# Kernel tuning notes

Hardware: AMD Instinct MI355X
Metric: run time of the kernel (lower is better)

## Reference

```python
import jax, jax.numpy as jnp
import numpy as np

T, V, E, H = 512, 32000, 512, 512

def setup_inputs() -> dict:
    key = jax.random.key(0)
    ks = jax.random.split(key, 6)
    return {
        "sent": jax.random.normal(ks[0], (T, V), dtype=jnp.float32),
        "W_e": jax.random.normal(ks[1], (E, V), dtype=jnp.float32),
        "W_x": jax.random.normal(ks[2], (H, E), dtype=jnp.float32),
        "W_h": jax.random.normal(ks[3], (H, H), dtype=jnp.float32),
        "W_p": jax.random.normal(ks[4], (V, H), dtype=jnp.float32),
        "b": jax.random.normal(ks[5], (H,), dtype=jnp.float32),
    }

def reference(sent, W_e, W_x, W_h, W_p, b):
    # Embed all input words at once (embed_word: W_e @ word), skip last token.
    emb = sent[:-1] @ W_e.T                 # [T-1, E]
    xproj = emb @ W_x.T + b                 # [T-1, H] (W_x @ e + b precomputed)

    def step(h_prev, xp):
        h = jax.nn.sigmoid(xp + W_h @ h_prev)  # elman_unit
        return h, h

    h0 = jnp.zeros((H,), dtype=jnp.float32)
    _, hs = jax.lax.scan(step, h0, xproj)   # [T-1, H]
    logits = hs @ W_p.T                     # [T-1, V]
    preds = jax.nn.softmax(logits, axis=-1) # softmax over vocab (dim=0 per step)
    return preds
```

## Files before the change

kernel.cpp:

```cpp
#include <hip/hip_runtime.h>
#include <math.h>

#define ROWS 511
#define VV   32000
#define HH   512

#define SLOTF   3584
#define DARRCAP 26112
#define TBL     520
#define MAXQ    17

__device__ __forceinline__ int pad4not8(int x) {
    int p = (x + 3) & ~3;
    if ((p & 7) == 0) p += 4;
    return p;
}
__device__ __forceinline__ int pad4(int x) { return (x + 3) & ~3; }

__device__ __forceinline__ int rfl(int x) { return __builtin_amdgcn_readfirstlane(x); }

__global__ __launch_bounds__(256) void gemm_nt(
    const float* __restrict__ A, const float* __restrict__ B, float* __restrict__ C,
    int M, int lda, int ldb, int ldc, int kChunk, int useAtomic)
{
    __shared__ float As[16][68];
    __shared__ float Bs[16][68];
    const int tid = threadIdx.x;
    const int bn = blockIdx.x, bm = blockIdx.y, bz = blockIdx.z;
    const int row = tid >> 2;
    const int seg = (tid & 3) << 2;
    const int tm  = (tid >> 4) << 2;
    const int tn  = (tid & 15) << 2;
    const int am = bm*64 + row;
    const size_t k0 = (size_t)bz * kChunk;
    const float* Ap = A + (size_t)am*lda + k0 + seg;
    const float* Bp = B + (size_t)(bn*64 + row)*ldb + k0 + seg;
    const bool aok = (am < M);
    float acc[4][4];
#pragma unroll
    for (int i=0;i<4;i++)
#pragma unroll
        for (int j=0;j<4;j++) acc[i][j]=0.f;

    for (int kt = 0; kt < kChunk; kt += 16) {
        float4 av = aok ? *(const float4*)(Ap + kt) : make_float4(0.f,0.f,0.f,0.f);
        float4 bv = *(const float4*)(Bp + kt);
        __syncthreads();
        As[seg+0][row]=av.x; As[seg+1][row]=av.y; As[seg+2][row]=av.z; As[seg+3][row]=av.w;
        Bs[seg+0][row]=bv.x; Bs[seg+1][row]=bv.y; Bs[seg+2][row]=bv.z; Bs[seg+3][row]=bv.w;
        __syncthreads();
#pragma unroll
        for (int k=0;k<16;k++){
            const float4 a  = *(const float4*)&As[k][tm];
            const float4 b4 = *(const float4*)&Bs[k][tn];
            float ar[4]={a.x,a.y,a.z,a.w};
            float br[4]={b4.x,b4.y,b4.z,b4.w};
#pragma unroll
            for (int i=0;i<4;i++)
#pragma unroll
                for (int j=0;j<4;j++)
                    acc[i][j] += ar[i]*br[j];
        }
    }
#pragma unroll
    for (int i=0;i<4;i++){
        int gm = bm*64 + tm + i;
        if (gm < M) {
            float* Cp = C + (size_t)gm*ldc + bn*64 + tn;
            if (useAtomic) {
                atomicAdd(Cp+0, acc[i][0]); atomicAdd(Cp+1, acc[i][1]);
                atomicAdd(Cp+2, acc[i][2]); atomicAdd(Cp+3, acc[i][3]);
            } else {
                *(float4*)Cp = make_float4(acc[i][0],acc[i][1],acc[i][2],acc[i][3]);
            }
        }
    }
}

__global__ __launch_bounds__(64) void rsum_kernel(const float* __restrict__ W_h, float* __restrict__ R)
{
    const int j = blockIdx.x;
    const int lane = threadIdx.x;
    float s = 0.f;
    for (int i = lane; i < HH; i += 64) s += fabsf(W_h[(size_t)j*HH + i]);
#pragma unroll
    for (int off = 32; off >= 1; off >>= 1) s += __shfl_down(s, off);
    if (lane == 0) R[j] = s;
}

__global__ __launch_bounds__(512) void classify_kernel(
    float* __restrict__ xp, const float* __restrict__ b, const float* __restrict__ R,
    float* __restrict__ Hm, int* __restrict__ idxJ, int* __restrict__ cnt)
{
    const int t = blockIdx.x;
    const int j = threadIdx.x;
    __shared__ int c;
    if (j == 0) c = 0;
    __syncthreads();
    float v = xp[(size_t)t*HH + j] + b[j];
    xp[(size_t)t*HH + j] = v;
    Hm[(size_t)t*HH + j] = (v > 0.f) ? 1.f : 0.f;
    if (fabsf(v) < R[j] + 30.0f) {
        int slot = atomicAdd(&c, 1);
        if (slot < 128) idxJ[t*128 + slot] = j;
    }
    __syncthreads();
    if (j == 0) cnt[t] = (c < 128) ? c : 128;
}

__global__ __launch_bounds__(512) void prefix_kernel(
    const int* __restrict__ cnt, int* __restrict__ offs, int* __restrict__ d4offs)
{
    __shared__ int sA[512];
    __shared__ int sB[512];
    const int t = threadIdx.x;
    int a = 0, b = 0;
    if (t >= 1 && t <= 510) a = cnt[t] * pad4not8(cnt[t-1]);
    if (t <= 510) b = pad4(cnt[t]);
    sA[t] = a; sB[t] = b;
    int va = a, vb = b;
    __syncthreads();
    for (int d = 1; d < 512; d <<= 1) {
        int ua = (t >= d) ? sA[t-d] : 0;
        int ub = (t >= d) ? sB[t-d] : 0;
        __syncthreads();
        va += ua; vb += ub;
        sA[t] = va; sB[t] = vb;
        __syncthreads();
    }
    if (t <= 510) offs[t] = va - a;
    d4offs[t] = vb - b;
}

__global__ __launch_bounds__(256) void gather_kernel(
    const float* __restrict__ W_h, const float* __restrict__ xp, const float* __restrict__ U,
    const int* __restrict__ idxJ, const int* __restrict__ cnt, const int* __restrict__ offs,
    float* __restrict__ wsub, int wsub_cap, float2* __restrict__ zs)
{
    const int t = blockIdx.x;
    const int cj = cnt[t];
    for (int jj = threadIdx.x; jj < cj; jj += 256) {
        int j = idxJ[t*128 + jj];
        float xpv = xp[(size_t)t*HH + j];
        float v = xpv;
        if (t > 0) v += U[(size_t)(t-1)*HH + j];
        zs[t*128 + jj] = make_float2(v, (xpv > 0.f) ? 1.f : 0.f);
    }
    if (t == 0) return;
    const int ci  = cnt[t-1];
    const int cip = pad4not8(ci);
    const int nw  = cj * cip;
    const int base = offs[t];
    if (base + nw > wsub_cap) return;
    for (int r = 0; r < cj; ++r) {
        const float* Wrow = W_h + (size_t)idxJ[t*128 + r] * HH;
        for (int c = threadIdx.x; c < cip; c += 256)
            wsub[base + r*cip + c] = (c < ci) ? Wrow[idxJ[(t-1)*128 + c]] : 0.f;
    }
}

__global__ __launch_bounds__(64, 1) void scan_kernel(
    const float2* __restrict__ zs, const int* __restrict__ idxJ,
    const int* __restrict__ cnt, const int* __restrict__ offs, const int* __restrict__ d4offs,
    const float* __restrict__ wsub, int wsub_cap,
    const float* __restrict__ W_h, float* __restrict__ Hm, float* __restrict__ darrg)
{
    __shared__ __align__(16) float  darr[DARRCAP];
    __shared__ __align__(16) float  db[2][132];
    __shared__ __align__(16) int4   rec[TBL];
    const int lane = threadIdx.x;
    const float* zsf = (const float*)zs;

    for (int i = lane; i < TBL; i += 64) {
        int c = (i < ROWS) ? cnt[i]    : 0;
        int o = (i < ROWS) ? offs[i]   : 0;
        int d = (i < ROWS) ? d4offs[i] : d4offs[511];
        rec[i] = make_int4(c, o, d, 0);
    }
    for (int i = lane * 4; i < DARRCAP; i += 256)
        *(float4*)&darr[i] = make_float4(0.f, 0.f, 0.f, 0.f);
    for (int i = lane; i < 132; i += 64) { db[0][i] = 0.f; db[1][i] = 0.f; }
    __syncthreads();

    const int  total   = rfl(rec[511].z);
    const bool useDarr = (total <= DARRCAP - 64);

    {
        const int cj0 = rfl(rec[0].x);
        for (int jj = lane; jj < cj0; jj += 64) {
            float2 zz = zs[jj];
            float h = 1.f / (1.f + __expf(-zz.x));
            float d = h - zz.y;
            if (useDarr) darr[jj] = d;
            else { db[0][jj] = d; Hm[idxJ[jj]] = h; }
        }
    }

    float4 W0[MAXQ], W1[MAXQ], W2[MAXQ];
    float2 z0, z1, z2;

    int ciP, sd4P;
    int cjC, sd4C, n4C; bool fastC;
    int cjN, sd4N, n4N; bool fastN;
    int cj2, wb2, sd42;

#define PF(CJPREV, CJT, WBT, BANK, ZB, TT, N4OUT, FASTOUT) do {                 \
        int cip_ = pad4not8(CJPREV);                                            \
        N4OUT = cip_ >> 2;                                                      \
        FASTOUT = ((CJT) <= 64) && (cip_ <= 68) &&                              \
                  ((long)(CJT) * cip_ <= SLOTF) && ((WBT) + SLOTF <= wsub_cap); \
        int row_ = min(lane, max((CJT) - 1, 0));                                \
        const float* gW_ = wsub + (FASTOUT ? ((WBT) + row_ * cip_) : 0);        \
        _Pragma("unroll")                                                       \
        for (int q = 0; q < MAXQ; ++q) {                                        \
            int off_ = (q < N4OUT) ? (q << 2) : 0;                              \
            BANK[q] = *(const float4*)(gW_ + off_);                             \
        }                                                                       \
        ZB = *(const float2*)&zsf[(size_t)(TT) * 256 + (lane << 1)];            \
    } while (0)

#define COMPUTE(TT, CURW, ZC) do {                                              \
        const float* dvec_ = useDarr ? &darr[sd4P] : db[((TT) - 1) & 1];        \
        if (fastC) {                                                            \
            if (lane < cjC) {                                                   \
                const float4* dr_ = (const float4*)dvec_;                       \
                float4 Dv[MAXQ];                                                \
                _Pragma("unroll")                                               \
                for (int g = 0; g < MAXQ; g += 4) {                             \
                    if (g < n4C) {                                              \
                        _Pragma("unroll")                                       \
                        for (int q = g; q < g + 4 && q < MAXQ; ++q)             \
                            Dv[q] = dr_[q];                                     \
                    }                                                           \
                }                                                               \
                float a0 = 0.f, a1 = 0.f, a2 = 0.f, a3 = 0.f;                   \
                _Pragma("unroll")                                               \
                for (int q = 0; q < MAXQ; ++q) {                                \
                    if (q < n4C) {                                              \
                        a0 += CURW[q].x * Dv[q].x; a1 += CURW[q].y * Dv[q].y;   \
                        a2 += CURW[q].z * Dv[q].z; a3 += CURW[q].w * Dv[q].w;   \
                    }                                                           \
                }                                                               \
                float z = ZC.x + (a0 + a1) + (a2 + a3);                         \
                float h = 1.f / (1.f + __expf(-z));                             \
                float d = h - ZC.y;                                             \
                if (useDarr) darr[sd4C + lane] = d;                             \
                else { db[(TT) & 1][lane] = d;                                  \
                       Hm[(size_t)(TT)*HH + idxJ[(TT)*128 + lane]] = h; }       \
            }                                                                   \
        } else {                                                                \
            for (int jj = lane; jj < cjC; jj += 64) {                           \
                int j = idxJ[(TT)*128 + jj];                                    \
                float2 zz = zs[(size_t)(TT)*128 + jj];                          \
                float zv = zz.x;                                                \
                for (int ii = 0; ii < ciP; ++ii)                                \
                    zv += W_h[(size_t)j*HH + idxJ[((TT)-1)*128 + ii]] * dvec_[ii]; \
                float h = 1.f / (1.f + __expf(-zv));                            \
                float dd = h - zz.y;                                            \
                if (useDarr) darr[sd4C + jj] = dd;                              \
                else { db[(TT) & 1][jj] = dd;                                   \
                       Hm[(size_t)(TT)*HH + j] = h; }                           \
            }                                                                   \
        }                                                                       \
    } while (0)

#define BODY(TT, PFB, ZPFB, CWB, ZCW) do {                                      \
        int n4p_; bool fp_;                                                     \
        PF(cjN, cj2, wb2, PFB, ZPFB, (TT) + 2, n4p_, fp_);                      \
        int4 rn3_ = rec[(TT) + 3];                                              \
        COMPUTE((TT), CWB, ZCW);                                                \
        ciP = cjC; sd4P = sd4C;                                                 \
        cjC = cjN; sd4C = sd4N; n4C = n4N; fastC = fastN;                       \
        cjN = cj2; sd4N = sd42; n4N = n4p_; fastN = fp_;                        \
        cj2 = rfl(rn3_.x); wb2 = rfl(rn3_.y); sd42 = rfl(rn3_.z);               \
    } while (0)

    ciP  = rfl(rec[0].x);
    sd4P = rfl(rec[0].z);
    {
        int cj1 = rfl(rec[1].x), wb1 = rfl(rec[1].y);
        cjC = cj1; sd4C = rfl(rec[1].z);
        PF(ciP, cj1, wb1, W1, z1, 1, n4C, fastC);
        int cjB = rfl(rec[2].x), wbB = rfl(rec[2].y);
        cjN = cjB; sd4N = rfl(rec[2].z);
        PF(cjC, cjB, wbB, W2, z2, 2, n4N, fastN);
        cj2 = rfl(rec[3].x); wb2 = rfl(rec[3].y); sd42 = rfl(rec[3].z);
    }

    for (int t = 1; t <= 510; t += 3) {
        BODY(t,     W0, z0, W1, z1);
        BODY(t + 1, W1, z1, W2, z2);
        BODY(t + 2, W2, z2, W0, z0);
    }

    if (useDarr) {
        for (int i = lane * 4; i < total; i += 256)
            *(float4*)&darrg[i] = *(float4*)&darr[i];
    }
#undef PF
#undef COMPUTE
#undef BODY
}

__global__ __launch_bounds__(64) void scatter_kernel(
    const float2* __restrict__ zs, const int* __restrict__ idxJ,
    const int* __restrict__ cnt, const int* __restrict__ d4offs,
    const float* __restrict__ darrg, float* __restrict__ Hm)
{
    if (d4offs[511] > DARRCAP - 64) return;
    const int t = blockIdx.x;
    const int c = cnt[t];
    for (int jj = threadIdx.x; jj < c; jj += 64)
        Hm[(size_t)t*HH + idxJ[t*128 + jj]] = zs[(size_t)t*128 + jj].y + darrg[d4offs[t] + jj];
}

__global__ __launch_bounds__(256) void softmax_kernel(float* __restrict__ out)
{
    const int row = blockIdx.x;
    const int tid = threadIdx.x;
    float* p = out + (size_t)row * VV;
    float m = -INFINITY, l = 0.f;
    for (int i = tid; i < VV; i += 256) {
        float x = p[i];
        if (x > m) { l = l * __expf(m - x) + 1.f; m = x; }
        else       { l += __expf(x - m); }
    }
#pragma unroll
    for (int off = 32; off >= 1; off >>= 1) {
        float m2 = __shfl_down(m, off);
        float l2 = __shfl_down(l, off);
        float M  = fmaxf(m, m2);
        l = l * __expf(m - M) + l2 * __expf(m2 - M);
        m = M;
    }
    __shared__ float sm[4], sl[4];
    const int wid = tid >> 6, lane = tid & 63;
    if (lane == 0) { sm[wid] = m; sl[wid] = l; }
    __syncthreads();
    if (tid == 0) {
        float M = sm[0], L = sl[0];
        for (int w = 1; w < 4; ++w) {
            float M2 = fmaxf(M, sm[w]);
            L = L * __expf(M - M2) + sl[w] * __expf(sm[w] - M2);
            M = M2;
        }
        sm[0] = M; sl[0] = 1.0f / L;
    }
    __syncthreads();
    const float M = sm[0], inv = sl[0];
    for (int i = tid; i < VV; i += 256) p[i] = __expf(p[i] - M) * inv;
}

extern "C" void kernel_launch(void* const* d_in, const int* in_sizes, int n_in,
                              void* d_out, int out_size, void* d_ws, size_t ws_size,
                              hipStream_t stream)
{
    const float* sent = (const float*)d_in[0];
    const float* W_e  = (const float*)d_in[1];
    const float* W_x  = (const float*)d_in[2];
    const float* W_h  = (const float*)d_in[3];
    const float* W_p  = (const float*)d_in[4];
    const float* b    = (const float*)d_in[5];
    float* out = (float*)d_out;
    float* ws  = (float*)d_ws;

    float*  emb    = ws;
    float*  xp     = ws + 262144;
    float*  U      = ws + 524288;
    float*  Hm     = ws + 786432;
    float*  R      = ws + 1048576;
    int*    cnt    = (int*)(ws + 1049088);
    int*    idxJ   = (int*)(ws + 1049600);
    int*    offs   = (int*)(ws + 1115136);
    int*    d4offs = (int*)(ws + 1115648);
    float2* zs     = (float2*)(ws + 1116160);
    float*  darrg  = ws + 1246976;
    float*  wsub   = ws + 1273088;
    long avail = (long)(ws_size / 4) - 1273088;
    int wsub_cap = (avail > 8388608L) ? 8388608 : (avail > 0 ? (int)avail : 0);

    hipMemsetAsync(ws, 0, (size_t)786432 * sizeof(float), stream);

    rsum_kernel<<<512, 64, 0, stream>>>(W_h, R);

    gemm_nt<<<dim3(8, 8, 8), 256, 0, stream>>>(sent, W_e, emb, ROWS, VV, VV, HH, 4000, 1);
    gemm_nt<<<dim3(8, 8, 4), 256, 0, stream>>>(emb, W_x, xp, ROWS, HH, HH, HH, 128, 1);

    classify_kernel<<<ROWS, 512, 0, stream>>>(xp, b, R, Hm, idxJ, cnt);

    gemm_nt<<<dim3(8, 8, 4), 256, 0, stream>>>(Hm, W_h, U, ROWS, HH, HH, HH, 128, 1);

    prefix_kernel<<<1, 512, 0, stream>>>(cnt, offs, d4offs);
    gather_kernel<<<ROWS, 256, 0, stream>>>(W_h, xp, U, idxJ, cnt, offs, wsub, wsub_cap, zs);
    scan_kernel<<<1, 64, 0, stream>>>(zs, idxJ, cnt, offs, d4offs, wsub, wsub_cap, W_h, Hm, darrg);
    scatter_kernel<<<ROWS, 64, 0, stream>>>(zs, idxJ, cnt, d4offs, darrg, Hm);

    gemm_nt<<<dim3(500, 8, 1), 256, 0, stream>>>(Hm, W_p, out, ROWS, HH, HH, VV, 512, 0);
    softmax_kernel<<<ROWS, 256, 0, stream>>>(out);
}
```

Before: 1.262 ms.

## Split scan dot products across four wavefronts with shared-memory partial sums

```diff
diff --git a/kernel.cpp b/kernel.cpp
--- a/kernel.cpp
+++ b/kernel.cpp
@@ -9,6 +9,7 @@
 #define DARRCAP 26112
 #define TBL     520
 #define MAXQ    17
+#define MAXQW   5
 
 __device__ __forceinline__ int pad4not8(int x) {
     int p = (x + 3) & ~3;
@@ -159,7 +160,7 @@
     }
 }
 
-__global__ __launch_bounds__(64, 1) void scan_kernel(
+__global__ __launch_bounds__(256, 1) void scan_kernel(
     const float2* __restrict__ zs, const int* __restrict__ idxJ,
     const int* __restrict__ cnt, const int* __restrict__ offs, const int* __restrict__ d4offs,
     const float* __restrict__ wsub, int wsub_cap,
@@ -168,18 +169,21 @@
     __shared__ __align__(16) float  darr[DARRCAP];
     __shared__ __align__(16) float  db[2][132];
     __shared__ __align__(16) int4   rec[TBL];
-    const int lane = threadIdx.x;
+    __shared__ float psum[2][4][72];
+    const int tid  = threadIdx.x;
+    const int wid  = tid >> 6;
+    const int lane = tid & 63;
     const float* zsf = (const float*)zs;
 
-    for (int i = lane; i < TBL; i += 64) {
+    for (int i = tid; i < TBL; i += 256) {
         int c = (i < ROWS) ? cnt[i]    : 0;
         int o = (i < ROWS) ? offs[i]   : 0;
         int d = (i < ROWS) ? d4offs[i] : d4offs[511];
         rec[i] = make_int4(c, o, d, 0);
     }
-    for (int i = lane * 4; i < DARRCAP; i += 256)
+    for (int i = tid * 4; i < DARRCAP; i += 1024)
         *(float4*)&darr[i] = make_float4(0.f, 0.f, 0.f, 0.f);
-    for (int i = lane; i < 132; i += 64) { db[0][i] = 0.f; db[1][i] = 0.f; }
+    for (int i = tid; i < 132; i += 256) { db[0][i] = 0.f; db[1][i] = 0.f; }
     __syncthreads();
 
     const int  total   = rfl(rec[511].z);
@@ -187,7 +191,7 @@
 
     {
         const int cj0 = rfl(rec[0].x);
-        for (int jj = lane; jj < cj0; jj += 64) {
+        for (int jj = tid; jj < cj0; jj += 256) {
             float2 zz = zs[jj];
             float h = 1.f / (1.f + __expf(-zz.x));
             float d = h - zz.y;
@@ -195,8 +199,9 @@
             else { db[0][jj] = d; Hm[idxJ[jj]] = h; }
         }
     }
-
-    float4 W0[MAXQ], W1[MAXQ], W2[MAXQ];
+    __syncthreads();
+
+    float4 W0[MAXQW], W1[MAXQW], W2[MAXQW];
     float2 z0, z1, z2;
 
     int ciP, sd4P;
@@ -212,9 +217,10 @@
         int row_ = min(lane, max((CJT) - 1, 0));                                \
         const float* gW_ = wsub + (FASTOUT ? ((WBT) + row_ * cip_) : 0);        \
         _Pragma("unroll")                                                       \
-        for (int q = 0; q < MAXQ; ++q) {                                        \
-            int off_ = (q < N4OUT) ? (q << 2) : 0;                              \
-            BANK[q] = *(const float4*)(gW_ + off_);                             \
+        for (int i = 0; i < MAXQW; ++i) {                                       \
+            int q_ = wid + 4 * i;                                               \
+            int off_ = (q_ < N4OUT) ? (q_ << 2) : 0;                            \
+            BANK[i] = *(const float4*)(gW_ + off_);                             \
         }                                                                       \
         ZB = *(const float2*)&zsf[(size_t)(TT) * 256 + (lane << 1)];            \
     } while (0)
@@ -222,34 +228,40 @@
 #define COMPUTE(TT, CURW, ZC) do {                                              \
         const float* dvec_ = useDarr ? &darr[sd4P] : db[((TT) - 1) & 1];        \
         if (fastC) {                                                            \
+            const float4* dr_ = (const float4*)dvec_;                           \
+            float4 Dv[MAXQW];                                                   \
+            _Pragma("unroll")                                                   \
+            for (int i = 0; i < MAXQW; ++i) {                                   \
+                int q_ = wid + 4 * i;                                           \
+                Dv[i] = dr_[(q_ < n4C) ? q_ : 0];                               \
+            }                                                                   \
+            float a0 = 0.f, a1 = 0.f, a2 = 0.f, a3 = 0.f;                       \
+            _Pragma("unroll")                                                   \
+            for (int i = 0; i < MAXQW; ++i) {                                   \
+                int q_ = wid + 4 * i;                                           \
+                if (q_ < n4C) {                                                 \
+                    a0 += CURW[i].x * Dv[i].x; a1 += CURW[i].y * Dv[i].y;       \
+                    a2 += CURW[i].z * Dv[i].z; a3 += CURW[i].w * Dv[i].w;       \
+                }                                                               \
+            }                                                                   \
+            psum[(TT) & 1][wid][lane] = (a0 + a1) + (a2 + a3);                  \
+            __asm__ __volatile__("s_waitcnt lgkmcnt(0)" ::: "memory");          \
+            __builtin_amdgcn_s_barrier();                                       \
             if (lane < cjC) {                                                   \
-                const float4* dr_ = (const float4*)dvec_;                       \
-                float4 Dv[MAXQ];                                                \
-                _Pragma("unroll")                                               \
-                for (int g = 0; g < MAXQ; g += 4) {                             \
-                    if (g < n4C) {                                              \
-                        _Pragma("unroll")                                       \
-                        for (int q = g; q < g + 4 && q < MAXQ; ++q)             \
-                            Dv[q] = dr_[q];                                     \
-                    }                                                           \
-                }                                                               \
-                float a0 = 0.f, a1 = 0.f, a2 = 0.f, a3 = 0.f;                   \
-                _Pragma("unroll")                                               \
-                for (int q = 0; q < MAXQ; ++q) {                                \
-                    if (q < n4C) {                                              \
-                        a0 += CURW[q].x * Dv[q].x; a1 += CURW[q].y * Dv[q].y;   \
-                        a2 += CURW[q].z * Dv[q].z; a3 += CURW[q].w * Dv[q].w;   \
-                    }                                                           \
-                }                                                               \
-                float z = ZC.x + (a0 + a1) + (a2 + a3);                         \
+                float p0 = psum[(TT) & 1][0][lane];                             \
+                float p1 = psum[(TT) & 1][1][lane];                             \
+                float p2 = psum[(TT) & 1][2][lane];                             \
+                float p3 = psum[(TT) & 1][3][lane];                             \
+                float z = ZC.x + ((p0 + p1) + (p2 + p3));                       \
                 float h = 1.f / (1.f + __expf(-z));                             \
                 float d = h - ZC.y;                                             \
                 if (useDarr) darr[sd4C + lane] = d;                             \
                 else { db[(TT) & 1][lane] = d;                                  \
-                       Hm[(size_t)(TT)*HH + idxJ[(TT)*128 + lane]] = h; }       \
+                       if (wid == 0)                                            \
+                           Hm[(size_t)(TT)*HH + idxJ[(TT)*128 + lane]] = h; }   \
             }                                                                   \
         } else {                                                                \
-            for (int jj = lane; jj < cjC; jj += 64) {                           \
+            for (int jj = tid; jj < cjC; jj += 256) {                           \
                 int j = idxJ[(TT)*128 + jj];                                    \
                 float2 zz = zs[(size_t)(TT)*128 + jj];                          \
                 float zv = zz.x;                                                \
@@ -261,6 +273,7 @@
                 else { db[(TT) & 1][jj] = dd;                                   \
                        Hm[(size_t)(TT)*HH + j] = h; }                           \
             }                                                                   \
+            __syncthreads();                                                    \
         }                                                                       \
     } while (0)
 
@@ -294,7 +307,7 @@
     }
 
     if (useDarr) {
-        for (int i = lane * 4; i < total; i += 256)
+        for (int i = tid * 4; i < total; i += 1024)
             *(float4*)&darrg[i] = *(float4*)&darr[i];
     }
 #undef PF
@@ -392,7 +405,7 @@
 
     prefix_kernel<<<1, 512, 0, stream>>>(cnt, offs, d4offs);
     gather_kernel<<<ROWS, 256, 0, stream>>>(W_h, xp, U, idxJ, cnt, offs, wsub, wsub_cap, zs);
-    scan_kernel<<<1, 64, 0, stream>>>(zs, idxJ, cnt, offs, d4offs, wsub, wsub_cap, W_h, Hm, darrg);
+    scan_kernel<<<1, 256, 0, stream>>>(zs, idxJ, cnt, offs, d4offs, wsub, wsub_cap, W_h, Hm, darrg);
     scatter_kernel<<<ROWS, 64, 0, stream>>>(zs, idxJ, cnt, d4offs, darrg, Hm);
 
     gemm_nt<<<dim3(500, 8, 1), 256, 0, stream>>>(Hm, W_p, out, ROWS, HH, HH, VV, 512, 0);
```

Result: faster. 1.224 ms (-3.0%).
